# Optimization experiments

Hardware: AMD Instinct MI355X
Metric: run time of the kernel (lower is better)

Reference implementation:

```python
import jax, jax.numpy as jnp
import numpy as np

K = 3; PAD = 1; CIN = 64; COUT = 64; B = 4; H = 128; W = 128


def setup_inputs() -> dict:
    key = jax.random.key(0)
    k1, k2, k3 = jax.random.split(key, 3)
    x = jax.random.normal(k1, (B, CIN, H, W), dtype=jnp.float32)
    # offset-predicting conv: [2*K*K, Cin, K, K]; small init -> sub-pixel offsets
    w_off = jax.random.normal(k2, (2 * K * K, CIN, K, K), dtype=jnp.float32) * 0.01
    b_off = jnp.zeros((2 * K * K,), dtype=jnp.float32)
    # deformable conv weight (bias=False): [Cout, Cin, K, K]
    w_def = jax.random.normal(k3, (COUT, CIN, K, K), dtype=jnp.float32) * 0.05
    return {"x": x, "w_off": w_off, "b_off": b_off, "w_def": w_def}


def _deform_conv(x, w_off, b_off, w_def):
    Bb, Cin, Hh, Ww = x.shape
    KK = K * K
    # 1) predict offsets with a regular 3x3 conv (stride 1, pad 1)
    off = jax.lax.conv_general_dilated(
        x, w_off, window_strides=(1, 1), padding=[(PAD, PAD), (PAD, PAD)],
        dimension_numbers=("NCHW", "OIHW", "NCHW"))
    off = off + b_off[None, :, None, None]          # [B, 2*KK, H, W]
    off = off.reshape(Bb, KK, 2, Hh, Ww)            # torchvision layout: (dy, dx) per tap
    dy, dx = off[:, :, 0], off[:, :, 1]             # [B, KK, H, W]

    # 2) sampling coordinates: p = p0 + p_k + offset
    ky = (jnp.arange(KK) // K).astype(x.dtype)
    kx = (jnp.arange(KK) % K).astype(x.dtype)
    hh = jnp.arange(Hh, dtype=x.dtype)
    ww = jnp.arange(Ww, dtype=x.dtype)
    py = hh[None, None, :, None] - PAD + ky[None, :, None, None] + dy   # [B,KK,H,W]
    px = ww[None, None, None, :] - PAD + kx[None, :, None, None] + dx

    # 3) bilinear sampling with zero padding outside the image
    y0f = jnp.floor(py); x0f = jnp.floor(px)
    fy = py - y0f; fx = px - x0f
    y0 = y0f.astype(jnp.int32); x0 = x0f.astype(jnp.int32)
    x_flat = x.reshape(Bb, Cin, Hh * Ww)

    def gather(yi, xi):
        valid = (yi >= 0) & (yi < Hh) & (xi >= 0) & (xi < Ww)
        idx = jnp.clip(yi, 0, Hh - 1) * Ww + jnp.clip(xi, 0, Ww - 1)     # [B,KK,H,W]
        g = jax.vmap(lambda xf, ix: xf[:, ix.reshape(-1)])(x_flat, idx)  # [B,Cin,KK*H*W]
        return g.reshape(Bb, Cin, KK, Hh, Ww) * valid[:, None].astype(x.dtype)

    sampled = (gather(y0, x0)         * ((1 - fy) * (1 - fx))[:, None]
             + gather(y0, x0 + 1)     * ((1 - fy) * fx)[:, None]
             + gather(y0 + 1, x0)     * (fy * (1 - fx))[:, None]
             + gather(y0 + 1, x0 + 1) * (fy * fx)[:, None])               # [B,Cin,KK,H,W]

    # 4) convolution accumulation over (Cin, kernel taps)
    return jnp.einsum('bckhw,ock->bohw', sampled, w_def.reshape(COUT, Cin, KK))


def reference(x, w_off, b_off, w_def):
    return _deform_conv(x, w_off, b_off, w_def)
```

## Files before the change

### kernel.cpp

```cpp
#include <hip/hip_runtime.h>
#include <hip/hip_fp16.h>

#define Bn   4
#define CINc 64
#define COUTc 64
#define Hn   128
#define Wn   128
#define HW   (Hn * Wn)
#define KKc  9
#define NOFF 18

typedef short bf16x8 __attribute__((ext_vector_type(8)));
typedef float f32x4  __attribute__((ext_vector_type(4)));
typedef float f32x2  __attribute__((ext_vector_type(2)));

__device__ inline unsigned short f2bf(float f) {
    unsigned int u = __float_as_uint(f);
    return (unsigned short)((u + 0x7fffu + ((u >> 16) & 1u)) >> 16);
}

__device__ inline void dma16(const void* g, void* l) {
#if __has_builtin(__builtin_amdgcn_global_load_lds)
    __builtin_amdgcn_global_load_lds(
        (__attribute__((address_space(1))) void*)(g),
        (__attribute__((address_space(3))) void*)(l), 16, 0, 0);
#else
    *(uint4*)l = *(const uint4*)g;
#endif
}

__global__ __launch_bounds__(256) void prep_all(
        const float* __restrict__ x, unsigned short* __restrict__ xt,
        const float* __restrict__ w_off, const float* __restrict__ w_def,
        unsigned short* __restrict__ wkb_sw, unsigned short* __restrict__ wob_sw) {
    int gb = blockIdx.x;
    int t  = threadIdx.x;
    if (gb < 1024) {
        __shared__ float s[64][65];
        int half = gb & 1;
        int h    = (gb >> 1) & 127;
        int b    = gb >> 8;
        int w0   = half * 64;
        int w = t & 63, cg = t >> 6;

        const float* xb = x + (size_t)b * CINc * HW + (size_t)h * Wn + w0 + w;
        #pragma unroll
        for (int i = 0; i < 16; ++i) {
            int c = cg * 16 + i;
            s[c][w] = xb[(size_t)c * HW];
        }
        __syncthreads();

        int cpair = t & 31, pxg = t >> 5;
        unsigned* xtp = (unsigned*)xt;
        #pragma unroll
        for (int i = 0; i < 8; ++i) {
            int px = pxg * 8 + i;
            float v0 = s[cpair * 2][px], v1 = s[cpair * 2 + 1][px];
            unsigned d = (unsigned)f2bf(v0) | ((unsigned)f2bf(v1) << 16);
            xtp[(((size_t)(b * Hn + h) * Wn) + w0 + px) * 32 + cpair] = d;
        }
        return;
    }
    int idx = (gb - 1024) * 256 + t;
    if (idx < 36864) {
        int j = idx & 7, l = (idx >> 3) & 63, s = idx >> 9;
        int k = s >> 3, kc = (s >> 2) & 1, ot = s & 3;
        int l15 = l & 15, quad = l >> 4;
        int o = ot * 16 + l15, c = kc * 32 + quad * 8 + j;
        wkb_sw[idx] = f2bf(w_def[((size_t)o * 64 + c) * 9 + k]);
    }
    int i2 = idx - 36864;
    if (i2 >= 0 && i2 < 18432) {
        int j = i2 & 7, l = (i2 >> 3) & 63, s = i2 >> 9;
        int tt = s >> 2, kc = (s >> 1) & 1, mt = s & 1;
        int l15 = l & 15, quad = l >> 4;
        int m = mt * 16 + l15, c = kc * 32 + quad * 8 + j;
        unsigned short v = 0;
        if (m < NOFF) v = f2bf(w_off[((size_t)m * 64 + c) * 9 + tt]);
        wob_sw[i2] = v;
    }
}

__global__ __launch_bounds__(512, 4) void fused_deform_v11(
        const unsigned short* __restrict__ xt,
        const unsigned short* __restrict__ wob_sw,
        const unsigned short* __restrict__ wkb_sw,
        const float* __restrict__ b_off, float* __restrict__ out) {
    __shared__ bf16x8 s_w[72 * 64];

    int gid  = blockIdx.x;
    int xcd  = gid & 7;
    int j    = gid >> 3;
    int hh   = j & 15;
    int b    = j >> 4;
    int h    = xcd * 16 + hh;
    int tid  = threadIdx.x;
    int lane = tid & 63;
    int wave = __builtin_amdgcn_readfirstlane(tid >> 6);
    int l15  = lane & 15;
    int quad = lane >> 4;
    int p    = wave * 16 + l15;

    #pragma unroll
    for (int i = 0; i < 5; ++i) {
        int seg = i * 8 + wave;
        if (seg < 36) {
            int ebase = seg * 64;
            dma16((const uint4*)wob_sw + ebase + lane,
                  (char*)s_w + (size_t)ebase * 16);
        }
    }

    uint4 L[9][2];
    unsigned msk[9];
    const unsigned short* xtb = xt + (size_t)b * HW * 64;
    #pragma unroll
    for (int t9 = 0; t9 < 9; ++t9) {
        int ty = t9 / 3, tx = t9 % 3;
        int y  = h - 1 + ty;
        int xg = p - 1 + tx;
        bool v = (y >= 0) && (y < Hn) && (xg >= 0) && (xg < Wn);
        msk[t9] = v ? 0xFFFFFFFFu : 0u;
        int yc = min(max(y, 0), Hn - 1);
        int xc = min(max(xg, 0), Wn - 1);
        size_t base = ((size_t)yc * Wn + xc) * 64;
        L[t9][0] = *(const uint4*)(xtb + base + quad * 8);
        L[t9][1] = *(const uint4*)(xtb + base + 32 + quad * 8);
    }
    __syncthreads();

    f32x4 oa0 = (f32x4){0.f, 0.f, 0.f, 0.f};
    f32x4 oa1 = (f32x4){0.f, 0.f, 0.f, 0.f};
    #pragma unroll
    for (int t9 = 0; t9 < 9; ++t9) {
        unsigned m = msk[t9];
        #pragma unroll
        for (int kc = 0; kc < 2; ++kc) {
            union { bf16x8 v; uint4 u; } bf;
            bf.u = L[t9][kc];
            bf.u.x &= m; bf.u.y &= m; bf.u.z &= m; bf.u.w &= m;
            bf16x8 a0 = s_w[((t9 * 2 + kc) * 2 + 0) * 64 + lane];
            bf16x8 a1 = s_w[((t9 * 2 + kc) * 2 + 1) * 64 + lane];
            oa0 = __builtin_amdgcn_mfma_f32_16x16x32_bf16(a0, bf.v, oa0, 0, 0, 0);
            oa1 = __builtin_amdgcn_mfma_f32_16x16x32_bf16(a1, bf.v, oa1, 0, 0, 0);
        }
    }

    unsigned my_ad[3]  = {0, 0, 0};
    unsigned my_w01[3] = {0, 0, 0};
    unsigned my_w23[3] = {0, 0, 0};
    auto phase1 = [&](int k, float dy, float dx, int slot) {
        float py  = (float)(h - 1 + k / 3) + dy;
        float pxf = (float)(p - 1 + k % 3) + dx;
        float y0f = floorf(py), x0f = floorf(pxf);
        float fy = py - y0f, fx = pxf - x0f;
        int y0 = (int)y0f, x0 = (int)x0f;
        bool vy0 = (y0 >= 0) & (y0 < Hn);
        bool vy1 = (y0 + 1 >= 0) & (y0 + 1 < Hn);
        bool vx0 = (x0 >= 0) & (x0 < Wn);
        bool vx1 = (x0 + 1 >= 0) & (x0 + 1 < Wn);
        float wy0 = vy0 ? 1.f - fy : 0.f;
        float wy1 = vy1 ? fy : 0.f;
        float wx0 = vx0 ? 1.f - fx : 0.f;
        float wx1 = vx1 ? fx : 0.f;
        int xc = min(max(x0, 0), Wn - 2);
        bool sel0 = (min(max(x0, 0), Wn - 1) != xc);
        bool sel1 = ((min(max(x0 + 1, 0), Wn - 1) - xc) == 1);
        float Wa = (sel0 ? 0.f : wx0) + (sel1 ? 0.f : wx1);
        float Wb = (sel0 ? wx0 : 0.f) + (sel1 ? wx1 : 0.f);
        int yc0 = min(max(y0, 0), Hn - 1), yc1 = min(max(y0 + 1, 0), Hn - 1);
        union { __half2 hv; unsigned u; } c01, c23;
        c01.hv = __floats2half2_rn(wy0 * Wa, wy0 * Wb);
        c23.hv = __floats2half2_rn(wy1 * Wa, wy1 * Wb);
        my_ad[slot]  = (unsigned)yc0 | ((unsigned)yc1 << 8) | ((unsigned)xc << 16);
        my_w01[slot] = c01.u;
        my_w23[slot] = c23.u;
    };
    int kb = quad * 2;
    phase1(kb,     oa0[0] + b_off[4 * quad],     oa0[1] + b_off[4 * quad + 1], 0);
    phase1(kb + 1, oa0[2] + b_off[4 * quad + 2], oa0[3] + b_off[4 * quad + 3], 1);
    if (quad == 0)
        phase1(8, oa1[0] + b_off[16], oa1[1] + b_off[17], 2);
    __syncthreads();

    #pragma unroll
    for (int i = 0; i < 9; ++i) {
        int seg = i * 8 + wave;
        int ebase = seg * 64;
        dma16((const uint4*)wkb_sw + ebase + lane,
              (char*)s_w + (size_t)ebase * 16);
    }

    unsigned at[KKc], ab[KKc];
    unsigned pw01[KKc], pw23[KKc];
    #pragma unroll
    for (int k = 0; k < KKc; ++k) {
        int src  = (k < 8) ? ((k >> 1) * 16 + l15) : l15;
        int slot = (k < 8) ? (k & 1) : 2;
        unsigned ad  = (unsigned)__shfl((int)my_ad[slot],  src, 64);
        pw01[k] = (unsigned)__shfl((int)my_w01[slot], src, 64);
        pw23[k] = (unsigned)__shfl((int)my_w23[slot], src, 64);
        int xc = (int)(ad >> 16);
        at[k] = (unsigned)(((ad & 255u) * Wn + xc) * 64);
        ab[k] = (unsigned)((((ad >> 8) & 255u) * Wn + xc) * 64);
    }
    __syncthreads();

    f32x4 acc[4];
    #pragma unroll
    for (int ot = 0; ot < 4; ++ot) acc[ot] = (f32x4){0.f, 0.f, 0.f, 0.f};

    uint4 R[2][8];
    int co0 = quad * 8, co1 = 32 + quad * 8;

    #define FETCH(kk, st)                                            \
        do {                                                         \
            R[st][0] = *(const uint4*)(xtb + at[kk] + co0);          \
            R[st][1] = *(const uint4*)(xtb + at[kk] + 64 + co0);     \
            R[st][2] = *(const uint4*)(xtb + ab[kk] + co0);          \
            R[st][3] = *(const uint4*)(xtb + ab[kk] + 64 + co0);     \
            R[st][4] = *(const uint4*)(xtb + at[kk] + co1);          \
            R[st][5] = *(const uint4*)(xtb + at[kk] + 64 + co1);     \
            R[st][6] = *(const uint4*)(xtb + ab[kk] + co1);          \
            R[st][7] = *(const uint4*)(xtb + ab[kk] + 64 + co1);     \
        } while (0)

    FETCH(0, 0);
    #pragma unroll
    for (int k = 0; k < KKc; ++k) {
        if (k < KKc - 1) FETCH(k + 1, (k + 1) & 1);
        const uint4* C = R[k & 1];
        union { unsigned u; __half2 hv; } c01, c23;
        c01.u = pw01[k]; c23.u = pw23[k];
        float W0 = __low2float(c01.hv), W1 = __high2float(c01.hv);
        float W2 = __low2float(c23.hv), W3 = __high2float(c23.hv);
        #pragma unroll
        for (int kc = 0; kc < 2; ++kc) {
            const unsigned* t0 = (const unsigned*)&C[kc * 4 + 0];
            const unsigned* t1 = (const unsigned*)&C[kc * 4 + 1];
            const unsigned* b0 = (const unsigned*)&C[kc * 4 + 2];
            const unsigned* b1 = (const unsigned*)&C[kc * 4 + 3];
            union { bf16x8 v; unsigned u[4]; } bf;
            #pragma unroll
            for (int jd = 0; jd < 4; ++jd) {
                f32x2 t0p = {__uint_as_float(t0[jd] << 16),
                             __uint_as_float(t0[jd] & 0xFFFF0000u)};
                f32x2 t1p = {__uint_as_float(t1[jd] << 16),
                             __uint_as_float(t1[jd] & 0xFFFF0000u)};
                f32x2 b0p = {__uint_as_float(b0[jd] << 16),
                             __uint_as_float(b0[jd] & 0xFFFF0000u)};
                f32x2 b1p = {__uint_as_float(b1[jd] << 16),
                             __uint_as_float(b1[jd] & 0xFFFF0000u)};
                f32x2 vv = t0p * W0 + t1p * W1 + b0p * W2 + b1p * W3;
                unsigned pk;
                asm("v_cvt_pk_bf16_f32 %0, %1, %2"
                    : "=v"(pk) : "v"(vv.x), "v"(vv.y));
                bf.u[jd] = pk;
            }
            #pragma unroll
            for (int ot = 0; ot < 4; ++ot) {
                bf16x8 af = s_w[((k * 2 + kc) * 4 + ot) * 64 + lane];
                acc[ot] = __builtin_amdgcn_mfma_f32_16x16x32_bf16(af, bf.v, acc[ot], 0, 0, 0);
            }
        }
    }
    #undef FETCH

    #pragma unroll
    for (int ot = 0; ot < 4; ++ot)
        #pragma unroll
        for (int r = 0; r < 4; ++r) {
            int o = ot * 16 + quad * 4 + r;
            out[(((size_t)b * COUTc + o) * Hn + h) * Wn + p] = acc[ot][r];
        }
}

extern "C" void kernel_launch(void* const* d_in, const int* in_sizes, int n_in,
                              void* d_out, int out_size, void* d_ws, size_t ws_size,
                              hipStream_t stream) {
    const float* x     = (const float*)d_in[0];
    const float* w_off = (const float*)d_in[1];
    const float* b_off = (const float*)d_in[2];
    const float* w_def = (const float*)d_in[3];
    float* out = (float*)d_out;

    char* ws = (char*)d_ws;
    unsigned short* xt = (unsigned short*)ws;
    ws += (size_t)Bn * HW * CINc * sizeof(unsigned short);
    unsigned short* wkb_sw = (unsigned short*)ws;
    ws += 36864 * sizeof(unsigned short);
    unsigned short* wob_sw = (unsigned short*)ws;

    prep_all<<<1024 + 216, 256, 0, stream>>>(x, xt, w_off, w_def, wkb_sw, wob_sw);
    fused_deform_v11<<<Bn * Hn, 512, 0, stream>>>(xt, wob_sw, wkb_sw, b_off, out);
}
```

Measured before the change: 117.0 us.

## Split output channels across two blocks and halve weight LDS footprint

Doubles the grid so each block computes 32 of the 64 output channels, with the deform weights re-laid out per half so only half the LDS is needed. Launch bounds rise to six blocks per CU and the offset-conv input loads are software-pipelined with a 4-slot ring instead of holding all 9 taps in registers. The cost is that each block recomputes the full offset convolution and bilinear sampling, doubling that work, in exchange for more parallelism and occupancy.

After: 154.4 us. 32.0% more time.

```diff
diff --git a/kernel.cpp b/kernel.cpp
--- a/kernel.cpp
+++ b/kernel.cpp
@@ -68,7 +68,9 @@
         int k = s >> 3, kc = (s >> 2) & 1, ot = s & 3;
         int l15 = l & 15, quad = l >> 4;
         int o = ot * 16 + l15, c = kc * 32 + quad * 8 + j;
-        wkb_sw[idx] = f2bf(w_def[((size_t)o * 64 + c) * 9 + k]);
+        int chh = ot >> 1, ot2 = ot & 1;
+        int dst = chh * 18432 + ((((k * 2 + kc) * 2) + ot2) << 9) + l * 8 + j;
+        wkb_sw[dst] = f2bf(w_def[((size_t)o * 64 + c) * 9 + k]);
     }
     int i2 = idx - 36864;
     if (i2 >= 0 && i2 < 18432) {
@@ -82,16 +84,18 @@
     }
 }
 
-__global__ __launch_bounds__(512, 4) void fused_deform_v11(
+__global__ __launch_bounds__(512, 6) void fused_deform_v12(
         const unsigned short* __restrict__ xt,
         const unsigned short* __restrict__ wob_sw,
         const unsigned short* __restrict__ wkb_sw,
         const float* __restrict__ b_off, float* __restrict__ out) {
-    __shared__ bf16x8 s_w[72 * 64];
+    __shared__ bf16x8 s_w[36 * 64];
 
     int gid  = blockIdx.x;
-    int xcd  = gid & 7;
-    int j    = gid >> 3;
+    int ch   = gid >> 9;
+    int g    = gid & 511;
+    int xcd  = g & 7;
+    int j    = g >> 3;
     int hh   = j & 15;
     int b    = j >> 4;
     int h    = xcd * 16 + hh;
@@ -112,40 +116,54 @@
         }
     }
 
-    uint4 L[9][2];
-    unsigned msk[9];
+    float4 bo  = ((const float4*)b_off)[quad];
+    float2 bo8 = ((const float2*)b_off)[8];
+
     const unsigned short* xtb = xt + (size_t)b * HW * 64;
-    #pragma unroll
-    for (int t9 = 0; t9 < 9; ++t9) {
-        int ty = t9 / 3, tx = t9 % 3;
-        int y  = h - 1 + ty;
-        int xg = p - 1 + tx;
-        bool v = (y >= 0) && (y < Hn) && (xg >= 0) && (xg < Wn);
-        msk[t9] = v ? 0xFFFFFFFFu : 0u;
-        int yc = min(max(y, 0), Hn - 1);
-        int xc = min(max(xg, 0), Wn - 1);
-        size_t base = ((size_t)yc * Wn + xc) * 64;
-        L[t9][0] = *(const uint4*)(xtb + base + quad * 8);
-        L[t9][1] = *(const uint4*)(xtb + base + 32 + quad * 8);
-    }
+    uint4 L[4][2];
+    unsigned msk4[4];
+    #define ISSUE(t9)                                                   \
+        do {                                                            \
+            int ty = (t9) / 3, tx = (t9) % 3;                           \
+            int y  = h - 1 + ty;                                        \
+            int xg = p - 1 + tx;                                        \
+            bool v = (y >= 0) && (y < Hn) && (xg >= 0) && (xg < Wn);    \
+            msk4[(t9) & 3] = v ? 0xFFFFFFFFu : 0u;                      \
+            int yc = min(max(y, 0), Hn - 1);                            \
+            int xc = min(max(xg, 0), Wn - 1);                           \
+            size_t base = ((size_t)yc * Wn + xc) * 64;                  \
+            L[(t9) & 3][0] = *(const uint4*)(xtb + base + quad * 8);    \
+            L[(t9) & 3][1] = *(const uint4*)(xtb + base + 32 + quad * 8); \
+        } while (0)
+    ISSUE(0); ISSUE(1); ISSUE(2); ISSUE(3);
     __syncthreads();
 
     f32x4 oa0 = (f32x4){0.f, 0.f, 0.f, 0.f};
     f32x4 oa1 = (f32x4){0.f, 0.f, 0.f, 0.f};
     #pragma unroll
     for (int t9 = 0; t9 < 9; ++t9) {
-        unsigned m = msk[t9];
+        unsigned m = msk4[t9 & 3];
         #pragma unroll
         for (int kc = 0; kc < 2; ++kc) {
             union { bf16x8 v; uint4 u; } bf;
-            bf.u = L[t9][kc];
+            bf.u = L[t9 & 3][kc];
             bf.u.x &= m; bf.u.y &= m; bf.u.z &= m; bf.u.w &= m;
             bf16x8 a0 = s_w[((t9 * 2 + kc) * 2 + 0) * 64 + lane];
             bf16x8 a1 = s_w[((t9 * 2 + kc) * 2 + 1) * 64 + lane];
             oa0 = __builtin_amdgcn_mfma_f32_16x16x32_bf16(a0, bf.v, oa0, 0, 0, 0);
             oa1 = __builtin_amdgcn_mfma_f32_16x16x32_bf16(a1, bf.v, oa1, 0, 0, 0);
         }
-    }
+        if (t9 < 5) {
+            switch (t9) {
+                case 0: ISSUE(4); break;
+                case 1: ISSUE(5); break;
+                case 2: ISSUE(6); break;
+                case 3: ISSUE(7); break;
+                case 4: ISSUE(8); break;
+            }
+        }
+    }
+    #undef ISSUE
 
     unsigned my_ad[3]  = {0, 0, 0};
     unsigned my_w01[3] = {0, 0, 0};
@@ -178,52 +196,55 @@
         my_w23[slot] = c23.u;
     };
     int kb = quad * 2;
-    phase1(kb,     oa0[0] + b_off[4 * quad],     oa0[1] + b_off[4 * quad + 1], 0);
-    phase1(kb + 1, oa0[2] + b_off[4 * quad + 2], oa0[3] + b_off[4 * quad + 3], 1);
+    phase1(kb,     oa0[0] + bo.x, oa0[1] + bo.y, 0);
+    phase1(kb + 1, oa0[2] + bo.z, oa0[3] + bo.w, 1);
     if (quad == 0)
-        phase1(8, oa1[0] + b_off[16], oa1[1] + b_off[17], 2);
+        phase1(8, oa1[0] + bo8.x, oa1[1] + bo8.y, 2);
     __syncthreads();
 
-    #pragma unroll
-    for (int i = 0; i < 9; ++i) {
+    const unsigned short* wkh = wkb_sw + (size_t)ch * 18432;
+    #pragma unroll
+    for (int i = 0; i < 5; ++i) {
         int seg = i * 8 + wave;
-        int ebase = seg * 64;
-        dma16((const uint4*)wkb_sw + ebase + lane,
-              (char*)s_w + (size_t)ebase * 16);
-    }
-
-    unsigned at[KKc], ab[KKc];
-    unsigned pw01[KKc], pw23[KKc];
+        if (seg < 36) {
+            int ebase = seg * 64;
+            dma16((const uint4*)wkh + ebase + lane,
+                  (char*)s_w + (size_t)ebase * 16);
+        }
+    }
+
+    unsigned ad[KKc], pw01[KKc], pw23[KKc];
     #pragma unroll
     for (int k = 0; k < KKc; ++k) {
         int src  = (k < 8) ? ((k >> 1) * 16 + l15) : l15;
         int slot = (k < 8) ? (k & 1) : 2;
-        unsigned ad  = (unsigned)__shfl((int)my_ad[slot],  src, 64);
+        ad[k]   = (unsigned)__shfl((int)my_ad[slot],  src, 64);
         pw01[k] = (unsigned)__shfl((int)my_w01[slot], src, 64);
         pw23[k] = (unsigned)__shfl((int)my_w23[slot], src, 64);
-        int xc = (int)(ad >> 16);
-        at[k] = (unsigned)(((ad & 255u) * Wn + xc) * 64);
-        ab[k] = (unsigned)((((ad >> 8) & 255u) * Wn + xc) * 64);
     }
     __syncthreads();
 
-    f32x4 acc[4];
-    #pragma unroll
-    for (int ot = 0; ot < 4; ++ot) acc[ot] = (f32x4){0.f, 0.f, 0.f, 0.f};
+    f32x4 acc[2];
+    acc[0] = (f32x4){0.f, 0.f, 0.f, 0.f};
+    acc[1] = (f32x4){0.f, 0.f, 0.f, 0.f};
 
     uint4 R[2][8];
     int co0 = quad * 8, co1 = 32 + quad * 8;
 
     #define FETCH(kk, st)                                            \
         do {                                                         \
-            R[st][0] = *(const uint4*)(xtb + at[kk] + co0);          \
-            R[st][1] = *(const uint4*)(xtb + at[kk] + 64 + co0);     \
-            R[st][2] = *(const uint4*)(xtb + ab[kk] + co0);          \
-            R[st][3] = *(const uint4*)(xtb + ab[kk] + 64 + co0);     \
-            R[st][4] = *(const uint4*)(xtb + at[kk] + co1);          \
-            R[st][5] = *(const uint4*)(xtb + at[kk] + 64 + co1);     \
-            R[st][6] = *(const uint4*)(xtb + ab[kk] + co1);          \
-            R[st][7] = *(const uint4*)(xtb + ab[kk] + 64 + co1);     \
+            unsigned ad_ = ad[kk];                                   \
+            unsigned xc_ = ad_ >> 16;                                \
+            unsigned at_ = (((ad_ & 255u) << 7) + xc_) << 6;         \
+            unsigned ab_ = ((((ad_ >> 8) & 255u) << 7) + xc_) << 6;  \
+            R[st][0] = *(const uint4*)(xtb + at_ + co0);             \
+            R[st][1] = *(const uint4*)(xtb + at_ + 64 + co0);        \
+            R[st][2] = *(const uint4*)(xtb + ab_ + co0);             \
+            R[st][3] = *(const uint4*)(xtb + ab_ + 64 + co0);        \
+            R[st][4] = *(const uint4*)(xtb + at_ + co1);             \
+            R[st][5] = *(const uint4*)(xtb + at_ + 64 + co1);        \
+            R[st][6] = *(const uint4*)(xtb + ab_ + co1);             \
+            R[st][7] = *(const uint4*)(xtb + ab_ + 64 + co1);        \
         } while (0)
 
     FETCH(0, 0);
@@ -259,20 +280,20 @@
                 bf.u[jd] = pk;
             }
             #pragma unroll
-            for (int ot = 0; ot < 4; ++ot) {
-                bf16x8 af = s_w[((k * 2 + kc) * 4 + ot) * 64 + lane];
-                acc[ot] = __builtin_amdgcn_mfma_f32_16x16x32_bf16(af, bf.v, acc[ot], 0, 0, 0);
+            for (int ot2 = 0; ot2 < 2; ++ot2) {
+                bf16x8 af = s_w[((k * 2 + kc) * 2 + ot2) * 64 + lane];
+                acc[ot2] = __builtin_amdgcn_mfma_f32_16x16x32_bf16(af, bf.v, acc[ot2], 0, 0, 0);
             }
         }
     }
     #undef FETCH
 
     #pragma unroll
-    for (int ot = 0; ot < 4; ++ot)
+    for (int ot2 = 0; ot2 < 2; ++ot2)
         #pragma unroll
         for (int r = 0; r < 4; ++r) {
-            int o = ot * 16 + quad * 4 + r;
-            out[(((size_t)b * COUTc + o) * Hn + h) * Wn + p] = acc[ot][r];
+            int o = ch * 32 + ot2 * 16 + quad * 4 + r;
+            out[(((size_t)b * COUTc + o) * Hn + h) * Wn + p] = acc[ot2][r];
         }
 }
 
@@ -293,5 +314,5 @@
     unsigned short* wob_sw = (unsigned short*)ws;
 
     prep_all<<<1024 + 216, 256, 0, stream>>>(x, xt, w_off, w_def, wkb_sw, wob_sw);
-    fused_deform_v11<<<Bn * Hn, 512, 0, stream>>>(xt, wob_sw, wkb_sw, b_off, out);
-}
+    fused_deform_v12<<<Bn * Hn * 2, 512, 0, stream>>>(xt, wob_sw, wkb_sw, b_off, out);
+}
```

## Split deformable-weight LDS staging into two halves to shrink shared memory

Applied to the files above, without the earlier changes.

The kernel now stages the deform-conv weights in LDS in two passes, first taps 0-3 and then taps 4-8, into a buffer of 40 segments instead of 72. The second DMA is issued while the bilinear B fragments for tap 4 are still being built, so the load overlaps with compute. The aim is to cut LDS use per block so more blocks fit on each CU, and to hide the weight load behind work. In exchange it adds an extra __syncthreads and a manually unrolled schedule, and the MFMA order inside each tap is interleaved across kc.

Result: no change. 115.5 us (-1.3%).

```diff
diff --git a/kernel.cpp b/kernel.cpp
--- a/kernel.cpp
+++ b/kernel.cpp
@@ -82,12 +82,58 @@
     }
 }
 
-__global__ __launch_bounds__(512, 4) void fused_deform_v11(
+
+#define BFBUILD(C, kc, BF, W0, W1, W2, W3)                                   \
+    do {                                                                     \
+        const unsigned* t0 = (const unsigned*)&(C)[(kc) * 4 + 0];            \
+        const unsigned* t1 = (const unsigned*)&(C)[(kc) * 4 + 1];            \
+        const unsigned* b0 = (const unsigned*)&(C)[(kc) * 4 + 2];            \
+        const unsigned* b1 = (const unsigned*)&(C)[(kc) * 4 + 3];            \
+        _Pragma("unroll")                                                    \
+        for (int jd = 0; jd < 4; ++jd) {                                     \
+            f32x2 t0p = {__uint_as_float(t0[jd] << 16),                      \
+                         __uint_as_float(t0[jd] & 0xFFFF0000u)};             \
+            f32x2 t1p = {__uint_as_float(t1[jd] << 16),                      \
+                         __uint_as_float(t1[jd] & 0xFFFF0000u)};             \
+            f32x2 b0p = {__uint_as_float(b0[jd] << 16),                      \
+                         __uint_as_float(b0[jd] & 0xFFFF0000u)};             \
+            f32x2 b1p = {__uint_as_float(b1[jd] << 16),                      \
+                         __uint_as_float(b1[jd] & 0xFFFF0000u)};             \
+            f32x2 vv = t0p * (W0) + t1p * (W1) + b0p * (W2) + b1p * (W3);    \
+            unsigned pk;                                                     \
+            asm("v_cvt_pk_bf16_f32 %0, %1, %2"                               \
+                : "=v"(pk) : "v"(vv.x), "v"(vv.y));                          \
+            (BF).u[jd] = pk;                                                 \
+        }                                                                    \
+    } while (0)
+
+#define TAP(k, SOFF)                                                         \
+    do {                                                                     \
+        const uint4* C = R[(k) & 1];                                         \
+        union { unsigned u; __half2 hv; } c01, c23;                          \
+        c01.u = pw01[(k)]; c23.u = pw23[(k)];                                \
+        float W0 = __low2float(c01.hv), W1 = __high2float(c01.hv);           \
+        float W2 = __low2float(c23.hv), W3 = __high2float(c23.hv);           \
+        union { bf16x8 v; unsigned u[4]; } bfa, bfb;                         \
+        BFBUILD(C, 0, bfa, W0, W1, W2, W3);                                  \
+        BFBUILD(C, 1, bfb, W0, W1, W2, W3);                                  \
+        _Pragma("unroll")                                                    \
+        for (int ot = 0; ot < 4; ++ot) {                                     \
+            bf16x8 af0 = s_w[(((k) * 2 + 0) * 4 + ot + (SOFF)) * 64 + lane]; \
+            acc[ot] = __builtin_amdgcn_mfma_f32_16x16x32_bf16(               \
+                af0, bfa.v, acc[ot], 0, 0, 0);                               \
+            bf16x8 af1 = s_w[(((k) * 2 + 1) * 4 + ot + (SOFF)) * 64 + lane]; \
+            acc[ot] = __builtin_amdgcn_mfma_f32_16x16x32_bf16(               \
+                af1, bfb.v, acc[ot], 0, 0, 0);                               \
+        }                                                                    \
+    } while (0)
+
+__global__ __launch_bounds__(512, 4) void fused_deform_v13(
         const unsigned short* __restrict__ xt,
         const unsigned short* __restrict__ wob_sw,
         const unsigned short* __restrict__ wkb_sw,
         const float* __restrict__ b_off, float* __restrict__ out) {
-    __shared__ bf16x8 s_w[72 * 64];
+    __shared__ bf16x8 s_w[40 * 64];
 
     int gid  = blockIdx.x;
     int xcd  = gid & 7;
@@ -185,11 +231,10 @@
     __syncthreads();
 
     #pragma unroll
-    for (int i = 0; i < 9; ++i) {
+    for (int i = 0; i < 4; ++i) {
         int seg = i * 8 + wave;
-        int ebase = seg * 64;
-        dma16((const uint4*)wkb_sw + ebase + lane,
-              (char*)s_w + (size_t)ebase * 16);
+        dma16((const uint4*)wkb_sw + (size_t)seg * 64 + lane,
+              (char*)s_w + (size_t)seg * 1024);
     }
 
     unsigned at[KKc], ab[KKc];
@@ -227,44 +272,44 @@
         } while (0)
 
     FETCH(0, 0);
-    #pragma unroll
-    for (int k = 0; k < KKc; ++k) {
-        if (k < KKc - 1) FETCH(k + 1, (k + 1) & 1);
-        const uint4* C = R[k & 1];
+    FETCH(1, 1); TAP(0, 0);
+    FETCH(2, 0); TAP(1, 0);
+    FETCH(3, 1); TAP(2, 0);
+    FETCH(4, 0); TAP(3, 0);
+    __syncthreads();
+
+    #pragma unroll
+    for (int i = 0; i < 5; ++i) {
+        int seg = i * 8 + wave;
+        dma16((const uint4*)wkb_sw + (size_t)(32 + seg) * 64 + lane,
+              (char*)s_w + (size_t)seg * 1024);
+    }
+
+    union { bf16x8 v; unsigned u[4]; } bf40, bf41;
+    {
+        const uint4* C = R[0];
         union { unsigned u; __half2 hv; } c01, c23;
-        c01.u = pw01[k]; c23.u = pw23[k];
+        c01.u = pw01[4]; c23.u = pw23[4];
         float W0 = __low2float(c01.hv), W1 = __high2float(c01.hv);
         float W2 = __low2float(c23.hv), W3 = __high2float(c23.hv);
-        #pragma unroll
-        for (int kc = 0; kc < 2; ++kc) {
-            const unsigned* t0 = (const unsigned*)&C[kc * 4 + 0];
-            const unsigned* t1 = (const unsigned*)&C[kc * 4 + 1];
-            const unsigned* b0 = (const unsigned*)&C[kc * 4 + 2];
-            const unsigned* b1 = (const unsigned*)&C[kc * 4 + 3];
-            union { bf16x8 v; unsigned u[4]; } bf;
-            #pragma unroll
-            for (int jd = 0; jd < 4; ++jd) {
-                f32x2 t0p = {__uint_as_float(t0[jd] << 16),
-                             __uint_as_float(t0[jd] & 0xFFFF0000u)};
-                f32x2 t1p = {__uint_as_float(t1[jd] << 16),
-                             __uint_as_float(t1[jd] & 0xFFFF0000u)};
-                f32x2 b0p = {__uint_as_float(b0[jd] << 16),
-                             __uint_as_float(b0[jd] & 0xFFFF0000u)};
-                f32x2 b1p = {__uint_as_float(b1[jd] << 16),
-                             __uint_as_float(b1[jd] & 0xFFFF0000u)};
-                f32x2 vv = t0p * W0 + t1p * W1 + b0p * W2 + b1p * W3;
-                unsigned pk;
-                asm("v_cvt_pk_bf16_f32 %0, %1, %2"
-                    : "=v"(pk) : "v"(vv.x), "v"(vv.y));
-                bf.u[jd] = pk;
-            }
-            #pragma unroll
-            for (int ot = 0; ot < 4; ++ot) {
-                bf16x8 af = s_w[((k * 2 + kc) * 4 + ot) * 64 + lane];
-                acc[ot] = __builtin_amdgcn_mfma_f32_16x16x32_bf16(af, bf.v, acc[ot], 0, 0, 0);
-            }
-        }
-    }
+        BFBUILD(C, 0, bf40, W0, W1, W2, W3);
+        BFBUILD(C, 1, bf41, W0, W1, W2, W3);
+    }
+    FETCH(5, 1);
+    __syncthreads();
+
+    #pragma unroll
+    for (int ot = 0; ot < 4; ++ot) {
+        bf16x8 af0 = s_w[(0 + ot) * 64 + lane];
+        acc[ot] = __builtin_amdgcn_mfma_f32_16x16x32_bf16(af0, bf40.v, acc[ot], 0, 0, 0);
+        bf16x8 af1 = s_w[(4 + ot) * 64 + lane];
+        acc[ot] = __builtin_amdgcn_mfma_f32_16x16x32_bf16(af1, bf41.v, acc[ot], 0, 0, 0);
+    }
+
+    FETCH(6, 0); TAP(5, -32);
+    FETCH(7, 1); TAP(6, -32);
+    FETCH(8, 0); TAP(7, -32);
+    TAP(8, -32);
     #undef FETCH
 
     #pragma unroll
@@ -293,5 +338,5 @@
     unsigned short* wob_sw = (unsigned short*)ws;
 
     prep_all<<<1024 + 216, 256, 0, stream>>>(x, xt, w_off, w_def, wkb_sw, wob_sw);
-    fused_deform_v11<<<Bn * Hn, 512, 0, stream>>>(xt, wob_sw, wkb_sw, b_off, out);
-}
+    fused_deform_v13<<<Bn * Hn, 512, 0, stream>>>(xt, wob_sw, wkb_sw, b_off, out);
+}
```
